# Kernel optimization log

Measured on AMD Instinct MI355X. Metric: run time of the kernel, lower is better.

The kernel has to match this reference:

```python
import jax, jax.numpy as jnp
import numpy as np

N_SEL = 8192      # total nodes across selected subgraphs
SUB_SZ = 32       # nodes per subgraph
N_SUB = 256       # number of subgraphs (N_SEL / SUB_SZ)
N_GRAPH = 64      # source graphs (4 subgraphs each)
N_FULL = 12288    # nodes in the full graph
E_RAW = 262144    # raw edges
N_PERS = 4        # weighted-cosine perspectives
D = 128           # feature dim
EPSILON = 0.1
LAMB1 = 0.5


def setup_inputs() -> dict:
    key = jax.random.key(0)
    k1, k2, k3, k4, k5 = jax.random.split(key, 5)
    x = jax.random.normal(k1, (N_SEL, D), dtype=jnp.float32)
    Wc = jax.random.normal(k2, (N_PERS, D), dtype=jnp.float32)
    selected_score = jax.random.uniform(k3, (N_SUB,), dtype=jnp.float32) + 0.1
    selected_batch = jnp.asarray(np.arange(N_SEL) // SUB_SZ, dtype=jnp.int32)
    selected_belong = jnp.asarray(np.arange(N_SUB) // (N_SUB // N_GRAPH), dtype=jnp.int32)
    # injective mapping from selected nodes -> full-graph node ids
    selected_mapping = jax.random.permutation(k4, N_FULL)[:N_SEL].astype(jnp.int32)
    # block-diagonal complete edge set within each subgraph (torch.meshgrid in prepare_parsed_data)
    base = (np.arange(N_SUB) * SUB_SZ)[:, None, None]
    r = np.broadcast_to(np.arange(SUB_SZ)[None, :, None], (N_SUB, SUB_SZ, SUB_SZ)) + base
    c = np.broadcast_to(np.arange(SUB_SZ)[None, None, :], (N_SUB, SUB_SZ, SUB_SZ)) + base
    full_edge_index = jnp.asarray(np.stack([r.ravel(), c.ravel()]), dtype=jnp.int32)
    raw_edge_index = jax.random.randint(k5, (2, E_RAW), 0, N_FULL, dtype=jnp.int32)
    return {"x": x, "Wc": Wc, "selected_score": selected_score,
            "selected_batch": selected_batch, "selected_mapping": selected_mapping,
            "selected_belong": selected_belong, "full_edge_index": full_edge_index,
            "raw_edge_index": raw_edge_index}


def reference(x, Wc, selected_score, selected_batch, selected_mapping,
              selected_belong, full_edge_index, raw_edge_index):
    # ---- per-graph scatter-normalization of subgraph scores ----
    score_sum = jax.ops.segment_sum(selected_score, selected_belong, num_segments=N_GRAPH)
    score = selected_score / score_sum[selected_belong]          # [N_SUB]

    # ---- WeightedCosine metric: dense pairwise adjacency over all selected nodes ----
    h = x[None, :, :] * Wc[:, None, :]                            # [P, N_sel, D]
    hn = h / jnp.clip(jnp.linalg.norm(h, axis=-1, keepdims=True), 1e-12)
    adj = jnp.einsum('pid,pjd->ij', hn, hn) / N_PERS              # [N_sel, N_sel]

    # ---- mask to intra-subgraph candidate edges ----
    mask = jnp.zeros((N_SEL, N_SEL), dtype=adj.dtype).at[full_edge_index[0], full_edge_index[1]].set(1.0)
    adj = adj * mask
    # EpsilonNN
    adj = adj * (adj > EPSILON).astype(adj.dtype)
    # RemoveSelfLoop
    adj = adj * (1.0 - jnp.eye(N_SEL, dtype=adj.dtype))
    # dense_to_sparse + weighting: weight each edge by its row-node's subgraph score
    attr = adj * (score[selected_batch] * LAMB1)[:, None]         # [N_sel, N_sel]

    # ---- map to full-graph ids and coalesce (duplicate-sum) into dense adjacency ----
    out = jnp.zeros((N_FULL, N_FULL), dtype=x.dtype)
    out = out.at[selected_mapping[:, None], selected_mapping[None, :]].add(attr)
    out = out.at[raw_edge_index[0], raw_edge_index[1]].add(1.0 - LAMB1)
    return out
```

## Files before the change

### kernel.cpp

```cpp
#include <hip/hip_runtime.h>

#define N_SEL 8192
#define SUB_SZ 32
#define N_SUB 256
#define N_GRAPH 64
#define N_FULL 12288
#define E_RAW 262144
#define N_PERS 4
#define D 128
#define EPSILON 0.1f
#define LAMB1 0.5f

#define N4_TOTAL 37748736
#define FILL_BLOCKS 4096
#define PER_BLOCK (N4_TOTAL / FILL_BLOCKS)
#define FILL_ITERS (PER_BLOCK / 256)

typedef float f4_t __attribute__((ext_vector_type(4)));

__global__ __launch_bounds__(256) void zero_kernel(f4_t* __restrict__ out)
{
    size_t base = (size_t)blockIdx.x * PER_BLOCK + threadIdx.x;
    const f4_t z = (f4_t){0.f, 0.f, 0.f, 0.f};
    #pragma unroll
    for (int k = 0; k < FILL_ITERS; ++k)
        __builtin_nontemporal_store(z, &out[base + (size_t)k * 256]);
}

__global__ __launch_bounds__(256) void scatter_kernel(
        const float* __restrict__ x,
        const float* __restrict__ Wc,
        const float* __restrict__ sscore,
        const int*   __restrict__ smap,
        const int*   __restrict__ rei,
        float* __restrict__ out)
{
    const int tid = threadIdx.x;

    if (blockIdx.x >= N_SUB) {
        int e = (blockIdx.x - N_SUB) * 256 + tid;
        long long r = rei[e];
        long long c = rei[E_RAW + e];
        atomicAdd(&out[r * (long long)N_FULL + c], 1.0f - LAMB1);
        return;
    }

    const int s    = blockIdx.x;
    const int base = s * SUB_SZ;

    __shared__ float xs[SUB_SZ][D + 1];
    __shared__ float w2[N_PERS][D];
    __shared__ float rnorm[N_PERS][SUB_SZ];
    __shared__ int   map_s[SUB_SZ];
    __shared__ float rowscore;

    for (int k = tid; k < SUB_SZ * D; k += 256) {
        int i = k >> 7;
        int d = k & (D - 1);
        xs[i][d] = x[(base + i) * D + d];
    }
    for (int k = tid; k < N_PERS * D; k += 256) {
        float w = Wc[k];
        ((float*)w2)[k] = w * w;
    }
    if (tid < SUB_SZ) map_s[tid] = smap[base + tid];
    if (tid == 0) {
        int g4 = (s >> 2) << 2;
        float sum = sscore[g4] + sscore[g4 + 1] + sscore[g4 + 2] + sscore[g4 + 3];
        rowscore = (sscore[s] / sum) * LAMB1;
    }
    __syncthreads();

    if (tid < N_PERS * SUB_SZ) {
        int p = tid >> 5;
        int i = tid & 31;
        float acc = 0.f;
        #pragma unroll 8
        for (int d = 0; d < D; ++d) {
            float v = xs[i][d];
            acc = fmaf(v * v, w2[p][d], acc);
        }
        rnorm[p][i] = 1.0f / fmaxf(sqrtf(acc), 1e-12f);
    }
    __syncthreads();

    for (int e = tid; e < SUB_SZ * SUB_SZ; e += 256) {
        int i = e >> 5;
        int j = e & 31;
        if (i == j) continue;
        float a0 = 0.f, a1 = 0.f, a2 = 0.f, a3 = 0.f;
        #pragma unroll 8
        for (int d = 0; d < D; ++d) {
            float prod = xs[i][d] * xs[j][d];
            a0 = fmaf(prod, w2[0][d], a0);
            a1 = fmaf(prod, w2[1][d], a1);
            a2 = fmaf(prod, w2[2][d], a2);
            a3 = fmaf(prod, w2[3][d], a3);
        }
        float adj = 0.25f * (a0 * rnorm[0][i] * rnorm[0][j] +
                             a1 * rnorm[1][i] * rnorm[1][j] +
                             a2 * rnorm[2][i] * rnorm[2][j] +
                             a3 * rnorm[3][i] * rnorm[3][j]);
        if (adj > EPSILON) {
            long long row = map_s[i];
            long long col = map_s[j];
            atomicAdd(&out[row * (long long)N_FULL + col], adj * rowscore);
        }
    }
}

extern "C" void kernel_launch(void* const* d_in, const int* in_sizes, int n_in,
                              void* d_out, int out_size, void* d_ws, size_t ws_size,
                              hipStream_t stream) {
    const float* x      = (const float*)d_in[0];
    const float* Wc     = (const float*)d_in[1];
    const float* sscore = (const float*)d_in[2];
    const int* smap = (const int*)d_in[4];
    const int* rei  = (const int*)d_in[7];
    float* out = (float*)d_out;

    zero_kernel<<<FILL_BLOCKS, 256, 0, stream>>>((f4_t*)out);

    scatter_kernel<<<N_SUB + E_RAW / 256, 256, 0, stream>>>(x, Wc, sscore, smap, rei, out);
}
```

Measured before the change: 160.3 us.

## Bucket edges per output chunk and build chunks in LDS before single streaming write

Global atomics into the huge dense output are replaced by appending (offset, value) pairs into per-chunk buckets in a workspace. A merge kernel then zeroes a 64KB chunk image in LDS, applies that chunk's entries with shared-memory atomics, and streams the chunk out with nontemporal stores. This fuses the zero fill with the scatter, so the output is written exactly once and scattered read-modify-write traffic to HBM is avoided. The cost is extra kernels, workspace traffic, 64KB LDS per block limiting occupancy, and entries silently dropped if a chunk exceeds 256 entries.

After: 168.5 us. 5.1% more time.

```diff
diff --git a/kernel.cpp b/kernel.cpp
--- a/kernel.cpp
+++ b/kernel.cpp
@@ -11,12 +11,146 @@
 #define EPSILON 0.1f
 #define LAMB1 0.5f
 
+#define CHUNK_FLOATS 16384
+#define N_CHUNKS 9216
+#define CAP 256
+#define WS_NEEDED ((size_t)N_CHUNKS * 4 + (size_t)N_CHUNKS * CAP * 8)
+
+typedef float f4_t __attribute__((ext_vector_type(4)));
+
+__global__ __launch_bounds__(256) void zero_counts_kernel(int* __restrict__ counts)
+{
+    int i = blockIdx.x * 256 + threadIdx.x;
+    if (i < N_CHUNKS) counts[i] = 0;
+}
+
+__device__ __forceinline__ void bucket_append(
+        int* counts, uint2* entries, long long flat, float v)
+{
+    int chunk = (int)(flat >> 14);
+    int local = (int)(flat & (CHUNK_FLOATS - 1));
+    int slot = atomicAdd(&counts[chunk], 1);
+    if (slot < CAP)
+        entries[(size_t)chunk * CAP + slot] = make_uint2((unsigned)local, __float_as_uint(v));
+}
+
+__global__ __launch_bounds__(256) void build_kernel(
+        const float* __restrict__ x,
+        const float* __restrict__ Wc,
+        const float* __restrict__ sscore,
+        const int*   __restrict__ smap,
+        const int*   __restrict__ rei,
+        int*   __restrict__ counts,
+        uint2* __restrict__ entries)
+{
+    const int tid = threadIdx.x;
+
+    if (blockIdx.x >= N_SUB) {
+        int e = (blockIdx.x - N_SUB) * 256 + tid;
+        long long r = rei[e];
+        long long c = rei[E_RAW + e];
+        bucket_append(counts, entries, r * (long long)N_FULL + c, 1.0f - LAMB1);
+        return;
+    }
+
+    const int s    = blockIdx.x;
+    const int base = s * SUB_SZ;
+
+    __shared__ float xs[SUB_SZ][D + 1];
+    __shared__ float w2[N_PERS][D];
+    __shared__ float rnorm[N_PERS][SUB_SZ];
+    __shared__ int   map_s[SUB_SZ];
+    __shared__ float rowscore;
+
+    for (int k = tid; k < SUB_SZ * D; k += 256) {
+        int i = k >> 7;
+        int d = k & (D - 1);
+        xs[i][d] = x[(base + i) * D + d];
+    }
+    for (int k = tid; k < N_PERS * D; k += 256) {
+        float w = Wc[k];
+        ((float*)w2)[k] = w * w;
+    }
+    if (tid < SUB_SZ) map_s[tid] = smap[base + tid];
+    if (tid == 0) {
+        int g4 = (s >> 2) << 2;
+        float sum = sscore[g4] + sscore[g4 + 1] + sscore[g4 + 2] + sscore[g4 + 3];
+        rowscore = (sscore[s] / sum) * LAMB1;
+    }
+    __syncthreads();
+
+    if (tid < N_PERS * SUB_SZ) {
+        int p = tid >> 5;
+        int i = tid & 31;
+        float acc = 0.f;
+        #pragma unroll 8
+        for (int d = 0; d < D; ++d) {
+            float v = xs[i][d];
+            acc = fmaf(v * v, w2[p][d], acc);
+        }
+        rnorm[p][i] = 1.0f / fmaxf(sqrtf(acc), 1e-12f);
+    }
+    __syncthreads();
+
+    for (int e = tid; e < SUB_SZ * SUB_SZ; e += 256) {
+        int i = e >> 5;
+        int j = e & 31;
+        if (i == j) continue;
+        float a0 = 0.f, a1 = 0.f, a2 = 0.f, a3 = 0.f;
+        #pragma unroll 8
+        for (int d = 0; d < D; ++d) {
+            float prod = xs[i][d] * xs[j][d];
+            a0 = fmaf(prod, w2[0][d], a0);
+            a1 = fmaf(prod, w2[1][d], a1);
+            a2 = fmaf(prod, w2[2][d], a2);
+            a3 = fmaf(prod, w2[3][d], a3);
+        }
+        float adj = 0.25f * (a0 * rnorm[0][i] * rnorm[0][j] +
+                             a1 * rnorm[1][i] * rnorm[1][j] +
+                             a2 * rnorm[2][i] * rnorm[2][j] +
+                             a3 * rnorm[3][i] * rnorm[3][j]);
+        if (adj > EPSILON) {
+            long long row = map_s[i];
+            long long col = map_s[j];
+            bucket_append(counts, entries, row * (long long)N_FULL + col, adj * rowscore);
+        }
+    }
+}
+
+__global__ __launch_bounds__(256) void fill_merge_kernel(
+        const int*   __restrict__ counts,
+        const uint2* __restrict__ entries,
+        float* __restrict__ out)
+{
+    __shared__ float img[CHUNK_FLOATS];
+    const int chunk = blockIdx.x;
+    const int tid   = threadIdx.x;
+    f4_t* img4 = (f4_t*)img;
+    const f4_t z = (f4_t){0.f, 0.f, 0.f, 0.f};
+
+    #pragma unroll
+    for (int k = 0; k < CHUNK_FLOATS / 4 / 256; ++k)
+        img4[tid + k * 256] = z;
+    __syncthreads();
+
+    int cnt = counts[chunk];
+    if (cnt > CAP) cnt = CAP;
+    for (int e = tid; e < cnt; e += 256) {
+        uint2 en = entries[(size_t)chunk * CAP + e];
+        atomicAdd(&img[en.x], __uint_as_float(en.y));
+    }
+    __syncthreads();
+
+    f4_t* out4 = (f4_t*)out + (size_t)chunk * (CHUNK_FLOATS / 4);
+    #pragma unroll
+    for (int k = 0; k < CHUNK_FLOATS / 4 / 256; ++k)
+        __builtin_nontemporal_store(img4[tid + k * 256], &out4[tid + k * 256]);
+}
+
 #define N4_TOTAL 37748736
 #define FILL_BLOCKS 4096
 #define PER_BLOCK (N4_TOTAL / FILL_BLOCKS)
 #define FILL_ITERS (PER_BLOCK / 256)
-
-typedef float f4_t __attribute__((ext_vector_type(4)));
 
 __global__ __launch_bounds__(256) void zero_kernel(f4_t* __restrict__ out)
 {
@@ -119,7 +253,17 @@
     const int* rei  = (const int*)d_in[7];
     float* out = (float*)d_out;
 
-    zero_kernel<<<FILL_BLOCKS, 256, 0, stream>>>((f4_t*)out);
-
-    scatter_kernel<<<N_SUB + E_RAW / 256, 256, 0, stream>>>(x, Wc, sscore, smap, rei, out);
-}
+    if (ws_size >= WS_NEEDED) {
+        int*   counts  = (int*)d_ws;
+        uint2* entries = (uint2*)((char*)d_ws + (size_t)N_CHUNKS * 4);
+
+        zero_counts_kernel<<<(N_CHUNKS + 255) / 256, 256, 0, stream>>>(counts);
+        build_kernel<<<N_SUB + E_RAW / 256, 256, 0, stream>>>(
+            x, Wc, sscore, smap, rei, counts, entries);
+        fill_merge_kernel<<<N_CHUNKS, 256, 0, stream>>>(counts, entries, out);
+    } else {
+        zero_kernel<<<FILL_BLOCKS, 256, 0, stream>>>((f4_t*)out);
+        scatter_kernel<<<N_SUB + E_RAW / 256, 256, 0, stream>>>(
+            x, Wc, sscore, smap, rei, out);
+    }
+}
```
